# Performance work log

Hardware: AMD Instinct MI355X
Metric: run time of the kernel (lower is better)

The kernel has to match this reference:

```python
import jax, jax.numpy as jnp
import numpy as np

MODES = 256
WIDTH = 64
T_HIST = 1
T_FUT = 1
BATCH = 64
S = 8192


def setup_inputs() -> dict:
    key = jax.random.key(0)
    ks = jax.random.split(key, 12)
    scale = 1.0 / (WIDTH * WIDTH)
    inp = {
        "u": jax.random.normal(ks[0], (BATCH, S, T_HIST), dtype=jnp.float32),
        # lifting layer: Linear(T_HIST+1 -> WIDTH), stored [in, out]
        "fc0_w": jax.random.normal(ks[1], (T_HIST + 1, WIDTH), dtype=jnp.float32) * 0.5,
        "fc0_b": jax.random.normal(ks[2], (WIDTH,), dtype=jnp.float32) * 0.1,
        # 4 spectral conv layers, complex weights stored as real/imag parts
        "sw_r": scale * jax.random.uniform(ks[3], (4, WIDTH, WIDTH, MODES), dtype=jnp.float32),
        "sw_i": scale * jax.random.uniform(ks[4], (4, WIDTH, WIDTH, MODES), dtype=jnp.float32),
        # 4 pointwise (1x1 conv) layers: weight [out,in], bias [out]
        "pw_w": jax.random.normal(ks[5], (4, WIDTH, WIDTH), dtype=jnp.float32) * (1.0 / np.sqrt(WIDTH)),
        "pw_b": jax.random.normal(ks[6], (4, WIDTH), dtype=jnp.float32) * 0.1,
        # projection head
        "fc1_w": jax.random.normal(ks[7], (WIDTH, 128), dtype=jnp.float32) * (1.0 / np.sqrt(WIDTH)),
        "fc1_b": jax.random.normal(ks[8], (128,), dtype=jnp.float32) * 0.1,
        "fc2_w": jax.random.normal(ks[9], (128, T_FUT), dtype=jnp.float32) * (1.0 / np.sqrt(128)),
        "fc2_b": jax.random.normal(ks[10], (T_FUT,), dtype=jnp.float32) * 0.1,
    }
    return inp


def _spectral_conv(x, wr, wi):
    # x: [b, c_in, s] real; weights: [c_in, c_out, MODES] (real/imag parts)
    s = x.shape[-1]
    xf = jnp.fft.rfft(x)                     # [b, c_in, s//2+1] complex
    w = wr + 1j * wi
    om = jnp.einsum('bix,iox->box', xf[:, :, :MODES], w)  # [b, c_out, MODES]
    out_ft = jnp.zeros((x.shape[0], wr.shape[1], s // 2 + 1), dtype=om.dtype)
    out_ft = out_ft.at[:, :, :MODES].set(om)
    return jnp.fft.irfft(out_ft, n=s)        # [b, c_out, s] real


def reference(u, fc0_w, fc0_b, sw_r, sw_i, pw_w, pw_b, fc1_w, fc1_b, fc2_w, fc2_b):
    b, s, _ = u.shape
    grid = jnp.broadcast_to(jnp.linspace(0.0, 1.0, s, dtype=u.dtype)[None, :, None], (b, s, 1))
    x = jnp.concatenate([u, grid], axis=-1)              # [b, s, 2]
    x = x @ fc0_w + fc0_b                                # [b, s, W]
    x = jnp.transpose(x, (0, 2, 1))                      # [b, W, s]
    for l in range(4):
        x1 = _spectral_conv(x, sw_r[l], sw_i[l])
        x2 = jnp.einsum('oi,bis->bos', pw_w[l], x) + pw_b[l][None, :, None]
        x = x1 + x2
        if l < 3:
            x = jax.nn.gelu(x, approximate=False)
    x = jnp.transpose(x, (0, 2, 1))                      # [b, s, W]
    x = jax.nn.gelu(x @ fc1_w + fc1_b, approximate=False)
    x = x @ fc2_w + fc2_b                                # [b, s, T_FUT]
    return x
```

## Files before the change

### kernel.cpp

```cpp
#include <hip/hip_runtime.h>
#include <hip/hip_bf16.h>
#include <math.h>

#define BB 64
#define CC 64
#define SS 8192
#define HS 4096
#define NMODE 256
#define KK2 512

typedef __attribute__((ext_vector_type(8))) short short8;
typedef __attribute__((ext_vector_type(16))) float f32x16;

__device__ __forceinline__ float gelu_exact(float v) {
    return 0.5f * v * (1.0f + erff(v * 0.7071067811865476f));
}
__device__ __forceinline__ float b2f(ushort u) {
    return __uint_as_float(((unsigned int)u) << 16);
}
__device__ __forceinline__ ushort f2b(float v) {
    __hip_bfloat16 h = __float2bfloat16(v);
    return *(ushort*)&h;
}
__device__ __forceinline__ void split2(float v, ushort& h, ushort& l) {
    h = f2b(v);
    l = f2b(v - b2f(h));
}
__device__ __forceinline__ int colk(int c) {
    return (c < 256) ? (c & ~1) : (((c - 256) & ~1) | 1);
}
__device__ __forceinline__ void dma16(const ushort* g, ushort* l) {
    __builtin_amdgcn_global_load_lds((const __attribute__((address_space(1))) void*)g,
                                     (__attribute__((address_space(3))) void*)l, 16, 0, 0);
}

__global__ void build_T1p(ushort* __restrict__ h, ushort* __restrict__ l) {
    int c = blockIdx.x;
    int n = blockIdx.y * 256 + threadIdx.x;
    int k = colk(c), ri = c & 1;
    int m = (n * k) & (SS - 1);
    float th = (float)m * (6.283185307179586476925f / (float)SS);
    float s, co;
    sincosf(th, &s, &co);
    float v = ri ? -s : co;
    ushort hh, ll;
    split2(v, hh, ll);
    h[(size_t)c * HS + n] = hh;
    l[(size_t)c * HS + n] = ll;
}

__global__ void build_T2r(ushort* __restrict__ h, ushort* __restrict__ l) {
    int n = blockIdx.x;
    int c = blockIdx.y * 256 + threadIdx.x;
    int k = colk(c), ri = c & 1;
    int m = (n * k) & (SS - 1);
    float th = (float)m * (6.283185307179586476925f / (float)SS);
    float s, co;
    sincosf(th, &s, &co);
    float v = ri ? -s : co;
    ushort hh, ll;
    split2(v, hh, ll);
    h[(size_t)n * KK2 + c] = hh;
    l[(size_t)n * KK2 + c] = ll;
}

__global__ void zero_xf(float* __restrict__ p) {
    size_t i = ((size_t)blockIdx.x * 256 + threadIdx.x) * 4;
    *(float4*)&p[i] = make_float4(0.f, 0.f, 0.f, 0.f);
}

__global__ void lift_kernel(const float* __restrict__ u, const float* __restrict__ w0,
                            const float* __restrict__ b0, ushort* __restrict__ Eh,
                            ushort* __restrict__ El, ushort* __restrict__ Oh,
                            ushort* __restrict__ Ol) {
    int n = blockIdx.x * 256 + threadIdx.x;
    int c = blockIdx.y;
    int b = blockIdx.z;
    float g1 = (float)n * (1.0f / (float)(SS - 1));
    float g2 = (float)(n + HS) * (1.0f / (float)(SS - 1));
    float v1 = u[b * SS + n] * w0[c] + g1 * w0[CC + c] + b0[c];
    float v2 = u[b * SS + n + HS] * w0[c] + g2 * w0[CC + c] + b0[c];
    float E = v1 + v2, O = v1 - v2;
    ushort hh, ll;
    size_t idx = (size_t)(b * CC + c) * HS + n;
    split2(E, hh, ll);
    Eh[idx] = hh;
    El[idx] = ll;
    split2(O, hh, ll);
    Oh[idx] = hh;
    Ol[idx] = ll;
}

__global__ __launch_bounds__(256, 3) void dft_mfma(
    const ushort* __restrict__ Eh, const ushort* __restrict__ El,
    const ushort* __restrict__ Oh, const ushort* __restrict__ Ol,
    const ushort* __restrict__ t1h, const ushort* __restrict__ t1l,
    float* __restrict__ Xf) {
    __shared__ __align__(16) ushort SM[16384];
    ushort* As_h = SM;
    ushort* As_l = SM + 4096;
    ushort* Bs_h = SM + 8192;
    ushort* Bs_l = SM + 12288;
    const int t = threadIdx.x;
    const int L = blockIdx.x;
    const int gq = L >> 5, j = L & 31;
    const int c0 = (j >> 3) * 128;
    const int m0 = ((gq & 3) * 8 + (j & 7)) * 128;
    const int kz = (gq >> 2) * 1024;
    const ushort* __restrict__ Ahp = (c0 < 256) ? Eh : Oh;
    const ushort* __restrict__ Alp = (c0 < 256) ? El : Ol;
    const int lane = t & 63, w = t >> 6;
    const int wm = (w >> 1) * 64, wn = (w & 1) * 64;
    const int l32 = lane & 31, lh = lane >> 5;
    const int sr = t >> 1, sh = (t & 1) * 16;
    const int g0 = (t & 1) * 2;
    const int d0 = ((g0 + 0) * 128 + sr) * 8;
    const int d1 = ((g0 + 1) * 128 + sr) * 8;

    f32x16 acc[2][2];
#pragma unroll
    for (int i = 0; i < 2; i++)
#pragma unroll
        for (int jj = 0; jj < 2; jj++) acc[i][jj] = (f32x16)0.f;

    const size_t arow = (size_t)(m0 + sr) * HS;
    const size_t brow = (size_t)(c0 + sr) * HS;
    const int kend = kz + 1024;

    short8 a0h, a1h, a0l, a1l, b0h, b1h, b0l, b1l;
    {
        const size_t ga = arow + kz + sh;
        const size_t gb = brow + kz + sh;
        a0h = *(const short8*)&Ahp[ga];
        a1h = *(const short8*)&Ahp[ga + 8];
        a0l = *(const short8*)&Alp[ga];
        a1l = *(const short8*)&Alp[ga + 8];
        b0h = *(const short8*)&t1h[gb];
        b1h = *(const short8*)&t1h[gb + 8];
        b0l = *(const short8*)&t1l[gb];
        b1l = *(const short8*)&t1l[gb + 8];
    }
    for (int kt = kz; kt < kend; kt += 32) {
        __syncthreads();
        *(short8*)&As_h[d0] = a0h;
        *(short8*)&As_h[d1] = a1h;
        *(short8*)&As_l[d0] = a0l;
        *(short8*)&As_l[d1] = a1l;
        *(short8*)&Bs_h[d0] = b0h;
        *(short8*)&Bs_h[d1] = b1h;
        *(short8*)&Bs_l[d0] = b0l;
        *(short8*)&Bs_l[d1] = b1l;
        __syncthreads();
        const int ktn = (kt + 32 < kend) ? kt + 32 : kz;
        const size_t ga = arow + ktn + sh;
        const size_t gb = brow + ktn + sh;
        a0h = *(const short8*)&Ahp[ga];
        a1h = *(const short8*)&Ahp[ga + 8];
        a0l = *(const short8*)&Alp[ga];
        a1l = *(const short8*)&Alp[ga + 8];
        b0h = *(const short8*)&t1h[gb];
        b1h = *(const short8*)&t1h[gb + 8];
        b0l = *(const short8*)&t1l[gb];
        b1l = *(const short8*)&t1l[gb + 8];
#pragma unroll
        for (int s2 = 0; s2 < 2; s2++) {
            const int kg = s2 * 2 + lh;
            short8 ah[2], al[2], bh2[2], bl2[2];
#pragma unroll
            for (int mt = 0; mt < 2; mt++) {
                int off = (kg * 128 + wm + mt * 32 + l32) * 8;
                ah[mt] = *(const short8*)&As_h[off];
                al[mt] = *(const short8*)&As_l[off];
            }
#pragma unroll
            for (int nt = 0; nt < 2; nt++) {
                int off = (kg * 128 + wn + nt * 32 + l32) * 8;
                bh2[nt] = *(const short8*)&Bs_h[off];
                bl2[nt] = *(const short8*)&Bs_l[off];
            }
#pragma unroll
            for (int nt = 0; nt < 2; nt++)
#pragma unroll
                for (int mt = 0; mt < 2; mt++) {
                    acc[mt][nt] = __builtin_amdgcn_mfma_f32_32x32x16_bf16(ah[mt], bh2[nt], acc[mt][nt], 0, 0, 0);
                    acc[mt][nt] = __builtin_amdgcn_mfma_f32_32x32x16_bf16(ah[mt], bl2[nt], acc[mt][nt], 0, 0, 0);
                    acc[mt][nt] = __builtin_amdgcn_mfma_f32_32x32x16_bf16(al[mt], bh2[nt], acc[mt][nt], 0, 0, 0);
                }
        }
    }
#pragma unroll
    for (int mt = 0; mt < 2; mt++)
#pragma unroll
        for (int nt = 0; nt < 2; nt++) {
            int col = c0 + wn + nt * 32 + l32;
#pragma unroll
            for (int reg = 0; reg < 16; reg++) {
                int row = m0 + wm + mt * 32 + (reg & 3) + 8 * (reg >> 2) + 4 * lh;
                atomicAdd(&Xf[(size_t)row * KK2 + col], acc[mt][nt][reg]);
            }
        }
}

__global__ __launch_bounds__(256) void mode_mix(const float* __restrict__ Xf,
                                                const float* __restrict__ swr,
                                                const float* __restrict__ swi,
                                                ushort* __restrict__ omh,
                                                ushort* __restrict__ oml, int l) {
    int k = threadIdx.x;
    int bg = blockIdx.x * 2;
    int og = blockIdx.y * 2;
    const int cp = ((k & 1) << 8) | ((k >> 1) << 1);
    float ar[2][2] = {}, ai[2][2] = {};
#pragma unroll 2
    for (int i = 0; i < CC; i++) {
        float2 x0 = *(const float2*)&Xf[((size_t)(bg + 0) * CC + i) * KK2 + cp];
        float2 x1 = *(const float2*)&Xf[((size_t)(bg + 1) * CC + i) * KK2 + cp];
        size_t wb = ((size_t)(l * CC + i) * CC + og) * NMODE + k;
        float wr0 = swr[wb], wi0 = swi[wb];
        float wr1 = swr[wb + NMODE], wi1 = swi[wb + NMODE];
        ar[0][0] += x0.x * wr0 - x0.y * wi0;
        ai[0][0] += x0.x * wi0 + x0.y * wr0;
        ar[0][1] += x0.x * wr1 - x0.y * wi1;
        ai[0][1] += x0.x * wi1 + x0.y * wr1;
        ar[1][0] += x1.x * wr0 - x1.y * wi0;
        ai[1][0] += x1.x * wi0 + x1.y * wr0;
        ar[1][1] += x1.x * wr1 - x1.y * wi1;
        ai[1][1] += x1.x * wi1 + x1.y * wr1;
    }
    float ck = (k == 0) ? (1.0f / (float)SS) : (2.0f / (float)SS);
#pragma unroll
    for (int b2 = 0; b2 < 2; b2++)
#pragma unroll
        for (int oo = 0; oo < 2; oo++) {
            float re = ar[b2][oo] * ck;
            float im = ai[b2][oo] * ck;
            ushort hr, lr2, hi2, li2;
            split2(re, hr, lr2);
            split2(im, hi2, li2);
            size_t base = ((size_t)(bg + b2) * CC + og + oo) * KK2 + cp;
            *(ushort2*)&omh[base] = make_ushort2(hr, hi2);
            *(ushort2*)&oml[base] = make_ushort2(lr2, li2);
        }
}

__global__ __launch_bounds__(256, 2) void inv_mfma(
    const ushort* __restrict__ omh, const ushort* __restrict__ oml,
    const ushort* __restrict__ t2h, const ushort* __restrict__ t2l,
    const float* __restrict__ pww, const float* __restrict__ pwb,
    ushort* __restrict__ Eh, ushort* __restrict__ El,
    ushort* __restrict__ Oh, ushort* __restrict__ Ol, int l, int gel) {
    __shared__ __align__(16) ushort SM[16384];
    ushort* As_h = SM;
    ushort* As_l = SM + 4096;
    ushort* Bs_h = SM + 8192;
    ushort* Bs_l = SM + 12288;
    const int t = threadIdx.x;
    const int n0 = blockIdx.x * 128;
    const int row0 = blockIdx.y * 128;
    const int lane = t & 63, w = t >> 6;
    const int wm = (w >> 1) * 64, wn = (w & 1) * 64;
    const int l32 = lane & 31, lh = lane >> 5;

    f32x16 aP[2][2], aQ[2][2];
#pragma unroll
    for (int i = 0; i < 2; i++)
#pragma unroll
        for (int jj = 0; jj < 2; jj++) {
            aP[i][jj] = (f32x16)0.f;
            aQ[i][jj] = (f32x16)0.f;
        }

    const size_t aoff = (size_t)(row0 + lane) * KK2 + w * 8;
    const size_t boff = (size_t)(n0 + lane) * KK2 + w * 8;
    const size_t rstep = (size_t)64 * KK2;
    ushort* dAh = As_h + w * 1024;
    ushort* dAl = As_l + w * 1024;
    ushort* dBh = Bs_h + w * 1024;
    ushort* dBl = Bs_l + w * 1024;

#pragma unroll
    for (int half = 0; half < 2; half++) {
        for (int hs8 = 0; hs8 < 8; hs8++) {
            const int kt = half * 256 + hs8 * 32;
            dma16(omh + aoff + kt, dAh);
            dma16(omh + aoff + rstep + kt, dAh + 512);
            dma16(oml + aoff + kt, dAl);
            dma16(oml + aoff + rstep + kt, dAl + 512);
            dma16(t2h + boff + kt, dBh);
            dma16(t2h + boff + rstep + kt, dBh + 512);
            dma16(t2l + boff + kt, dBl);
            dma16(t2l + boff + rstep + kt, dBl + 512);
            __syncthreads();
#pragma unroll
            for (int s2 = 0; s2 < 2; s2++) {
                const int kg = s2 * 2 + lh;
                short8 ah[2], al[2], bh2[2], bl2[2];
#pragma unroll
                for (int mt = 0; mt < 2; mt++) {
                    int off = (kg * 128 + wm + mt * 32 + l32) * 8;
                    ah[mt] = *(const short8*)&As_h[off];
                    al[mt] = *(const short8*)&As_l[off];
                }
#pragma unroll
                for (int nt = 0; nt < 2; nt++) {
                    int off = (kg * 128 + wn + nt * 32 + l32) * 8;
                    bh2[nt] = *(const short8*)&Bs_h[off];
                    bl2[nt] = *(const short8*)&Bs_l[off];
                }
#pragma unroll
                for (int nt = 0; nt < 2; nt++)
#pragma unroll
                    for (int mt = 0; mt < 2; mt++) {
                        f32x16* ac = half ? &aQ[mt][nt] : &aP[mt][nt];
                        *ac = __builtin_amdgcn_mfma_f32_32x32x16_bf16(ah[mt], bh2[nt], *ac, 0, 0, 0);
                        *ac = __builtin_amdgcn_mfma_f32_32x32x16_bf16(ah[mt], bl2[nt], *ac, 0, 0, 0);
                        *ac = __builtin_amdgcn_mfma_f32_32x32x16_bf16(al[mt], bh2[nt], *ac, 0, 0, 0);
                    }
            }
            __syncthreads();
        }
    }
#pragma unroll
    for (int mt = 0; mt < 2; mt++)
#pragma unroll
        for (int nt = 0; nt < 2; nt++) {
            f32x16 p = aP[mt][nt];
            aP[mt][nt] = p + aQ[mt][nt];
            aQ[mt][nt] = p - aQ[mt][nt];
        }
    short8 pah[4][2], pal[4][2];
#pragma unroll
    for (int ks = 0; ks < 4; ks++)
#pragma unroll
        for (int mt = 0; mt < 2; mt++) {
            const float* pp = &pww[(size_t)(l * CC + mt * 32 + l32) * CC + ks * 16 + lh * 8];
            float4 pa = *(const float4*)pp;
            float4 pb = *(const float4*)(pp + 4);
            float pv[8] = {pa.x, pa.y, pa.z, pa.w, pb.x, pb.y, pb.z, pb.w};
#pragma unroll
            for (int e = 0; e < 8; e++) {
                ushort h2, l2;
                split2(0.5f * pv[e], h2, l2);
                pah[ks][mt][e] = (short)h2;
                pal[ks][mt][e] = (short)l2;
            }
        }
    const size_t xsrc = (size_t)(row0 + (w >> 1) * 64 + (w & 1) * 32 + (lane >> 4)) * HS +
                        n0 + (lane & 15) * 8;
    ushort* dX = SM + w * 4096;
    const int bsw = w >> 1;
    const ushort* const srcs[4] = {Eh, El, Oh, Ol};
#pragma unroll
    for (int r = 0; r < 4; r++) {
        const ushort* src = srcs[r];
        const bool isO = (r >= 2), isHi = !(r & 1);
        __syncthreads();
#pragma unroll
        for (int q = 0; q < 8; q++) dma16(src + xsrc + (size_t)q * 4 * HS, dX + q * 512);
        __syncthreads();
#pragma unroll
        for (int ks = 0; ks < 4; ks++) {
            short8 bf[2], nbf[2];
#pragma unroll
            for (int nt = 0; nt < 2; nt++) {
                const int rb = (bsw * 64 + ks * 16 + lh * 8) * 128 + wn + nt * 32 + l32;
#pragma unroll
                for (int jj = 0; jj < 8; jj++) bf[nt][jj] = (short)SM[rb + jj * 128];
                if (isO) {
#pragma unroll
                    for (int jj = 0; jj < 8; jj++)
                        nbf[nt][jj] = (short)(bf[nt][jj] ^ (short)0x8000);
                }
            }
#pragma unroll
            for (int nt = 0; nt < 2; nt++)
#pragma unroll
                for (int mt = 0; mt < 2; mt++) {
                    aP[mt][nt] = __builtin_amdgcn_mfma_f32_32x32x16_bf16(pah[ks][mt], bf[nt], aP[mt][nt], 0, 0, 0);
                    aQ[mt][nt] = __builtin_amdgcn_mfma_f32_32x32x16_bf16(pah[ks][mt], isO ? nbf[nt] : bf[nt], aQ[mt][nt], 0, 0, 0);
                    if (isHi) {
                        aP[mt][nt] = __builtin_amdgcn_mfma_f32_32x32x16_bf16(pal[ks][mt], bf[nt], aP[mt][nt], 0, 0, 0);
                        aQ[mt][nt] = __builtin_amdgcn_mfma_f32_32x32x16_bf16(pal[ks][mt], isO ? nbf[nt] : bf[nt], aQ[mt][nt], 0, 0, 0);
                    }
                }
        }
    }
#pragma unroll
    for (int mt = 0; mt < 2; mt++)
#pragma unroll
        for (int nt = 0; nt < 2; nt++)
#pragma unroll
            for (int reg = 0; reg < 16; reg++) {
                int roffs = (reg & 3) + 8 * (reg >> 2) + 4 * lh;
                float bias = pwb[l * CC + mt * 32 + roffs];
                float uu = aP[mt][nt][reg] + bias;
                float vv = aQ[mt][nt][reg] + bias;
                if (gel) {
                    uu = gelu_exact(uu);
                    vv = gelu_exact(vv);
                }
                float EE = uu + vv, OO = uu - vv;
                ushort h2, l2;
                size_t gg = (size_t)(row0 + wm + mt * 32 + roffs) * HS + n0 + wn + nt * 32 + l32;
                split2(EE, h2, l2);
                Eh[gg] = h2;
                El[gg] = l2;
                split2(OO, h2, l2);
                Oh[gg] = h2;
                Ol[gg] = l2;
            }
}

__global__ __launch_bounds__(256, 3) void head_kernel(
    const ushort* __restrict__ Eh, const ushort* __restrict__ El,
    const ushort* __restrict__ Oh, const ushort* __restrict__ Ol,
    const float* __restrict__ w1, const float* __restrict__ b1,
    const float* __restrict__ w2, const float* __restrict__ b2,
    float* __restrict__ out) {
    __shared__ __align__(16) ushort Xh[4096];
    __shared__ __align__(16) ushort Xl[4096];
    __shared__ __align__(16) ushort Wh[8192];
    __shared__ __align__(16) ushort Wl[8192];
    __shared__ float part[4][64];
    const int b = blockIdx.y;
    const int n0 = blockIdx.x * 64;
    const int t = threadIdx.x;
    const int lane = t & 63, w = t >> 6;
    const int l32 = lane & 31, lh = lane >> 5;
    const float sg = (n0 < HS) ? 0.5f : -0.5f;
    const int nc = n0 & (HS - 1);
    {
        const int n = lane;
        const size_t gx = (size_t)(b * CC + w * 16) * HS + nc + n;
        short8 fh[2], fl[2];
#pragma unroll
        for (int cc = 0; cc < 16; cc++) {
            size_t g = gx + (size_t)cc * HS;
            float e = b2f(Eh[g]) + b2f(El[g]);
            float o = b2f(Oh[g]) + b2f(Ol[g]);
            float x = 0.5f * e + sg * o;
            ushort hh, ll;
            split2(x, hh, ll);
            fh[cc >> 3][cc & 7] = (short)hh;
            fl[cc >> 3][cc & 7] = (short)ll;
        }
        const int kg0 = w * 2;
#pragma unroll
        for (int q = 0; q < 2; q++) {
            *(short8*)&Xh[((kg0 + q) * 64 + n) * 8] = fh[q];
            *(short8*)&Xl[((kg0 + q) * 64 + n) * 8] = fl[q];
        }
    }
    {
        const int j = t & 127, half = t >> 7;
#pragma unroll
        for (int q = 0; q < 4; q++) {
            const int kg = half * 4 + q;
            short8 fh, fl;
#pragma unroll
            for (int e = 0; e < 8; e++) {
                int c = kg * 8 + e;
                ushort hh, ll;
                split2(w1[c * 128 + j], hh, ll);
                fh[e] = (short)hh;
                fl[e] = (short)ll;
            }
            *(short8*)&Wh[(kg * 128 + j) * 8] = fh;
            *(short8*)&Wl[(kg * 128 + j) * 8] = fl;
        }
    }
    __syncthreads();
    f32x16 acc[2];
    acc[0] = (f32x16)0.f;
    acc[1] = (f32x16)0.f;
#pragma unroll
    for (int ks = 0; ks < 4; ks++) {
        const int kg = ks * 2 + lh;
        const int offa = (kg * 128 + w * 32 + l32) * 8;
        short8 awh = *(const short8*)&Wh[offa];
        short8 awl = *(const short8*)&Wl[offa];
#pragma unroll
        for (int nt = 0; nt < 2; nt++) {
            const int offb = (kg * 64 + nt * 32 + l32) * 8;
            short8 bxh = *(const short8*)&Xh[offb];
            short8 bxl = *(const short8*)&Xl[offb];
            acc[nt] = __builtin_amdgcn_mfma_f32_32x32x16_bf16(awh, bxh, acc[nt], 0, 0, 0);
            acc[nt] = __builtin_amdgcn_mfma_f32_32x32x16_bf16(awh, bxl, acc[nt], 0, 0, 0);
            acc[nt] = __builtin_amdgcn_mfma_f32_32x32x16_bf16(awl, bxh, acc[nt], 0, 0, 0);
        }
    }
#pragma unroll
    for (int nt = 0; nt < 2; nt++) {
        float s = 0.f;
#pragma unroll
        for (int reg = 0; reg < 16; reg++) {
            const int j0 = w * 32 + (reg & 3) + 8 * (reg >> 2) + 4 * lh;
            s += gelu_exact(acc[nt][reg] + b1[j0]) * w2[j0];
        }
        s += __shfl_xor(s, 32);
        part[w][nt * 32 + l32] = s;
    }
    __syncthreads();
    if (t < 64)
        out[b * SS + n0 + t] = part[0][t] + part[1][t] + part[2][t] + part[3][t] + b2[0];
}

extern "C" void kernel_launch(void* const* d_in, const int* in_sizes, int n_in,
                              void* d_out, int out_size, void* d_ws, size_t ws_size,
                              hipStream_t stream) {
    (void)in_sizes; (void)n_in; (void)out_size; (void)ws_size;
    const float* u = (const float*)d_in[0];
    const float* fc0_w = (const float*)d_in[1];
    const float* fc0_b = (const float*)d_in[2];
    const float* sw_r = (const float*)d_in[3];
    const float* sw_i = (const float*)d_in[4];
    const float* pw_w = (const float*)d_in[5];
    const float* pw_b = (const float*)d_in[6];
    const float* fc1_w = (const float*)d_in[7];
    const float* fc1_b = (const float*)d_in[8];
    const float* fc2_w = (const float*)d_in[9];
    const float* fc2_b = (const float*)d_in[10];
    float* out = (float*)d_out;

    char* ws = (char*)d_ws;
    ushort* Eh = (ushort*)ws;
    ushort* El = (ushort*)(ws + 33554432);
    ushort* Oh = (ushort*)(ws + 67108864);
    ushort* Ol = (ushort*)(ws + 100663296);
    ushort* t1h = (ushort*)(ws + 134217728);
    ushort* t1l = (ushort*)(ws + 138412032);
    ushort* t2h = (ushort*)(ws + 142606336);
    ushort* t2l = (ushort*)(ws + 146800640);
    ushort* omh = (ushort*)(ws + 150994944);
    ushort* oml = (ushort*)(ws + 155189248);
    float* Xf = (float*)(ws + 159383552);

    build_T1p<<<dim3(KK2, HS / 256), 256, 0, stream>>>(t1h, t1l);
    build_T2r<<<dim3(HS, KK2 / 256), 256, 0, stream>>>(t2h, t2l);
    lift_kernel<<<dim3(HS / 256, CC, BB), 256, 0, stream>>>(u, fc0_w, fc0_b, Eh, El,
                                                            Oh, Ol);
    for (int l = 0; l < 4; l++) {
        zero_xf<<<dim3(2048), 256, 0, stream>>>(Xf);
        dft_mfma<<<dim3(512), 256, 0, stream>>>(Eh, El, Oh, Ol, t1h, t1l, Xf);
        mode_mix<<<dim3(BB / 2, CC / 2), 256, 0, stream>>>(Xf, sw_r, sw_i, omh, oml, l);
        inv_mfma<<<dim3(HS / 128, 32), 256, 0, stream>>>(
            omh, oml, t2h, t2l, pw_w, pw_b, Eh, El, Oh, Ol, l, (l < 3) ? 1 : 0);
    }
    head_kernel<<<dim3(SS / 64, BB), 256, 0, stream>>>(Eh, El, Oh, Ol, fc1_w, fc1_b,
                                                       fc2_w, fc2_b, out);
}
```

Measured before the change: 1.269 ms.

## Double-buffer LDS staging in inv_mfma to overlap global loads with MFMA

```diff
diff --git a/kernel.cpp b/kernel.cpp
--- a/kernel.cpp
+++ b/kernel.cpp
@@ -11,6 +11,10 @@
 
 typedef __attribute__((ext_vector_type(8))) short short8;
 typedef __attribute__((ext_vector_type(16))) float f32x16;
+
+#define VMW8 asm volatile("s_waitcnt vmcnt(8)" ::: "memory")
+#define VMW0 asm volatile("s_waitcnt vmcnt(0)" ::: "memory")
+#define SBAR asm volatile("s_barrier" ::: "memory")
 
 __device__ __forceinline__ float gelu_exact(float v) {
     return 0.5f * v * (1.0f + erff(v * 0.7071067811865476f));
@@ -249,11 +253,7 @@
     const float* __restrict__ pww, const float* __restrict__ pwb,
     ushort* __restrict__ Eh, ushort* __restrict__ El,
     ushort* __restrict__ Oh, ushort* __restrict__ Ol, int l, int gel) {
-    __shared__ __align__(16) ushort SM[16384];
-    ushort* As_h = SM;
-    ushort* As_l = SM + 4096;
-    ushort* Bs_h = SM + 8192;
-    ushort* Bs_l = SM + 12288;
+    __shared__ __align__(16) ushort SM[32768];
     const int t = threadIdx.x;
     const int n0 = blockIdx.x * 128;
     const int row0 = blockIdx.y * 128;
@@ -273,52 +273,84 @@
     const size_t aoff = (size_t)(row0 + lane) * KK2 + w * 8;
     const size_t boff = (size_t)(n0 + lane) * KK2 + w * 8;
     const size_t rstep = (size_t)64 * KK2;
-    ushort* dAh = As_h + w * 1024;
-    ushort* dAl = As_l + w * 1024;
-    ushort* dBh = Bs_h + w * 1024;
-    ushort* dBl = Bs_l + w * 1024;
-
-#pragma unroll
-    for (int half = 0; half < 2; half++) {
-        for (int hs8 = 0; hs8 < 8; hs8++) {
-            const int kt = half * 256 + hs8 * 32;
-            dma16(omh + aoff + kt, dAh);
-            dma16(omh + aoff + rstep + kt, dAh + 512);
-            dma16(oml + aoff + kt, dAl);
-            dma16(oml + aoff + rstep + kt, dAl + 512);
-            dma16(t2h + boff + kt, dBh);
-            dma16(t2h + boff + rstep + kt, dBh + 512);
-            dma16(t2l + boff + kt, dBl);
-            dma16(t2l + boff + rstep + kt, dBl + 512);
-            __syncthreads();
-#pragma unroll
-            for (int s2 = 0; s2 < 2; s2++) {
-                const int kg = s2 * 2 + lh;
-                short8 ah[2], al[2], bh2[2], bl2[2];
+
+    auto stage1 = [&](int st, int bsel) {
+        const int kt = st * 32;
+        ushort* base = SM + bsel * 16384;
+        ushort* dAh = base + w * 1024;
+        ushort* dAl = base + 4096 + w * 1024;
+        ushort* dBh = base + 8192 + w * 1024;
+        ushort* dBl = base + 12288 + w * 1024;
+        dma16(omh + aoff + kt, dAh);
+        dma16(omh + aoff + rstep + kt, dAh + 512);
+        dma16(oml + aoff + kt, dAl);
+        dma16(oml + aoff + rstep + kt, dAl + 512);
+        dma16(t2h + boff + kt, dBh);
+        dma16(t2h + boff + rstep + kt, dBh + 512);
+        dma16(t2l + boff + kt, dBl);
+        dma16(t2l + boff + rstep + kt, dBl + 512);
+    };
+    const size_t xsrc = (size_t)(row0 + (w >> 1) * 64 + (w & 1) * 32 + (lane >> 4)) * HS +
+                        n0 + (lane & 15) * 8;
+    auto stage2 = [&](const ushort* src, int bsel) {
+        ushort* dX = SM + bsel * 16384 + w * 4096;
+#pragma unroll
+        for (int q = 0; q < 8; q++) dma16(src + xsrc + (size_t)q * 4 * HS, dX + q * 512);
+    };
+    auto compute1 = [&](f32x16 (&acc)[2][2], const int bsel) {
+        const ushort* base = SM + bsel * 16384;
+#pragma unroll
+        for (int s2 = 0; s2 < 2; s2++) {
+            const int kg = s2 * 2 + lh;
+            short8 ah[2], al[2], bh2[2], bl2[2];
+#pragma unroll
+            for (int mt = 0; mt < 2; mt++) {
+                int off = (kg * 128 + wm + mt * 32 + l32) * 8;
+                ah[mt] = *(const short8*)&base[off];
+                al[mt] = *(const short8*)&base[4096 + off];
+            }
+#pragma unroll
+            for (int nt = 0; nt < 2; nt++) {
+                int off = (kg * 128 + wn + nt * 32 + l32) * 8;
+                bh2[nt] = *(const short8*)&base[8192 + off];
+                bl2[nt] = *(const short8*)&base[12288 + off];
+            }
+#pragma unroll
+            for (int nt = 0; nt < 2; nt++)
 #pragma unroll
                 for (int mt = 0; mt < 2; mt++) {
-                    int off = (kg * 128 + wm + mt * 32 + l32) * 8;
-                    ah[mt] = *(const short8*)&As_h[off];
-                    al[mt] = *(const short8*)&As_l[off];
+                    acc[mt][nt] = __builtin_amdgcn_mfma_f32_32x32x16_bf16(ah[mt], bh2[nt], acc[mt][nt], 0, 0, 0);
+                    acc[mt][nt] = __builtin_amdgcn_mfma_f32_32x32x16_bf16(ah[mt], bl2[nt], acc[mt][nt], 0, 0, 0);
+                    acc[mt][nt] = __builtin_amdgcn_mfma_f32_32x32x16_bf16(al[mt], bh2[nt], acc[mt][nt], 0, 0, 0);
                 }
-#pragma unroll
-                for (int nt = 0; nt < 2; nt++) {
-                    int off = (kg * 128 + wn + nt * 32 + l32) * 8;
-                    bh2[nt] = *(const short8*)&Bs_h[off];
-                    bl2[nt] = *(const short8*)&Bs_l[off];
-                }
-#pragma unroll
-                for (int nt = 0; nt < 2; nt++)
-#pragma unroll
-                    for (int mt = 0; mt < 2; mt++) {
-                        f32x16* ac = half ? &aQ[mt][nt] : &aP[mt][nt];
-                        *ac = __builtin_amdgcn_mfma_f32_32x32x16_bf16(ah[mt], bh2[nt], *ac, 0, 0, 0);
-                        *ac = __builtin_amdgcn_mfma_f32_32x32x16_bf16(ah[mt], bl2[nt], *ac, 0, 0, 0);
-                        *ac = __builtin_amdgcn_mfma_f32_32x32x16_bf16(al[mt], bh2[nt], *ac, 0, 0, 0);
-                    }
-            }
-            __syncthreads();
-        }
+        }
+    };
+
+    stage1(0, 0);
+#pragma unroll 1
+    for (int st = 0; st < 8; st++) {
+        const int buf = st & 1;
+        stage1(st + 1, buf ^ 1);
+        VMW8;
+        SBAR;
+        compute1(aP, buf);
+        SBAR;
+    }
+#pragma unroll 1
+    for (int st = 8; st < 15; st++) {
+        const int buf = st & 1;
+        stage1(st + 1, buf ^ 1);
+        VMW8;
+        SBAR;
+        compute1(aQ, buf);
+        SBAR;
+    }
+    {
+        stage2(Eh, 0);
+        VMW8;
+        SBAR;
+        compute1(aQ, 1);
+        SBAR;
     }
 #pragma unroll
     for (int mt = 0; mt < 2; mt++)
@@ -345,19 +377,20 @@
                 pal[ks][mt][e] = (short)l2;
             }
         }
-    const size_t xsrc = (size_t)(row0 + (w >> 1) * 64 + (w & 1) * 32 + (lane >> 4)) * HS +
-                        n0 + (lane & 15) * 8;
-    ushort* dX = SM + w * 4096;
     const int bsw = w >> 1;
     const ushort* const srcs[4] = {Eh, El, Oh, Ol};
 #pragma unroll
     for (int r = 0; r < 4; r++) {
-        const ushort* src = srcs[r];
+        const int buf = r & 1;
         const bool isO = (r >= 2), isHi = !(r & 1);
-        __syncthreads();
-#pragma unroll
-        for (int q = 0; q < 8; q++) dma16(src + xsrc + (size_t)q * 4 * HS, dX + q * 512);
-        __syncthreads();
+        if (r < 3) {
+            stage2(srcs[r + 1], buf ^ 1);
+            VMW8;
+        } else {
+            VMW0;
+        }
+        SBAR;
+        const ushort* base = SM + buf * 16384;
 #pragma unroll
         for (int ks = 0; ks < 4; ks++) {
             short8 bf[2], nbf[2];
@@ -365,7 +398,7 @@
             for (int nt = 0; nt < 2; nt++) {
                 const int rb = (bsw * 64 + ks * 16 + lh * 8) * 128 + wn + nt * 32 + l32;
 #pragma unroll
-                for (int jj = 0; jj < 8; jj++) bf[nt][jj] = (short)SM[rb + jj * 128];
+                for (int jj = 0; jj < 8; jj++) bf[nt][jj] = (short)base[rb + jj * 128];
                 if (isO) {
 #pragma unroll
                     for (int jj = 0; jj < 8; jj++)
@@ -384,6 +417,7 @@
                     }
                 }
         }
+        if (r < 3) SBAR;
     }
 #pragma unroll
     for (int mt = 0; mt < 2; mt++)
```

After: 1.281 ms. About the same (+0.9%).
